# Performance work log

Hardware: AMD Instinct MI355X
Metric: run time of the kernel (lower is better)

Reference implementation:

```python
import jax, jax.numpy as jnp
import numpy as np

B, T, E, H = 2, 2048, 1024, 16
HS = E // H  # head size = 64
EPS = 1e-5


def setup_inputs() -> dict:
    key = jax.random.key(0)
    ks = jax.random.split(key, 12)
    s_e = 1.0 / np.sqrt(E)
    s_4e = 1.0 / np.sqrt(4 * E)
    return {
        "x": jax.random.normal(ks[0], (B, T, E), dtype=jnp.float32),
        # per-head projections (no bias), stacked over heads: [H, E, HS]
        "Wq": jax.random.uniform(ks[1], (H, E, HS), jnp.float32, -s_e, s_e),
        "Wk": jax.random.uniform(ks[2], (H, E, HS), jnp.float32, -s_e, s_e),
        "Wv": jax.random.uniform(ks[3], (H, E, HS), jnp.float32, -s_e, s_e),
        # output projection
        "Wo": jax.random.uniform(ks[4], (E, E), jnp.float32, -s_e, s_e),
        "bo": jax.random.uniform(ks[5], (E,), jnp.float32, -s_e, s_e),
        # feed-forward
        "W1": jax.random.uniform(ks[6], (E, 4 * E), jnp.float32, -s_e, s_e),
        "b1": jax.random.uniform(ks[7], (4 * E,), jnp.float32, -s_e, s_e),
        "W2": jax.random.uniform(ks[8], (4 * E, E), jnp.float32, -s_4e, s_4e),
        "b2": jax.random.uniform(ks[9], (E,), jnp.float32, -s_4e, s_4e),
        # layernorms
        "g1": jnp.ones((E,), jnp.float32),
        "be1": jnp.zeros((E,), jnp.float32),
        "g2": jnp.ones((E,), jnp.float32),
        "be2": jnp.zeros((E,), jnp.float32),
    }


def _layernorm(x, g, b):
    mu = jnp.mean(x, axis=-1, keepdims=True)
    var = jnp.var(x, axis=-1, keepdims=True)
    return (x - mu) * jax.lax.rsqrt(var + EPS) * g + b


def reference(x, Wq, Wk, Wv, Wo, bo, W1, b1, W2, b2, g1, be1, g2, be2):
    Bx, Tx, Ex = x.shape
    # --- multi-head causal self-attention (dropout = identity in eval) ---
    q = jnp.einsum("bte,hed->bhtd", x, Wq)
    k = jnp.einsum("bte,hed->bhtd", x, Wk)
    v = jnp.einsum("bte,hed->bhtd", x, Wv)
    scale = HS ** -0.5
    scores = jnp.einsum("bhtd,bhsd->bhts", q, k) * scale  # [B,H,T,T]
    causal = jnp.tril(jnp.ones((Tx, Tx), dtype=bool))
    scores = jnp.where(causal, scores, -jnp.inf)
    att = jax.nn.softmax(scores, axis=-1)
    out = jnp.einsum("bhts,bhsd->bhtd", att, v)  # [B,H,T,HS]
    out = out.transpose(0, 2, 1, 3).reshape(Bx, Tx, Ex)  # concat heads
    out = out @ Wo + bo
    # --- residual + LN1 ---
    x = _layernorm(x + out, g1, be1)
    # --- feed-forward ---
    h = jax.nn.relu(x @ W1 + b1)
    ff = h @ W2 + b2
    # --- residual + LN2 ---
    return _layernorm(x + ff, g2, be2)
```

## Files before the change

kernel.cpp:

```cpp
#include <hip/hip_runtime.h>
#include <hip/hip_bf16.h>
#include <cstdint>
#include <cstddef>

typedef __hip_bfloat16 bf16;
typedef __attribute__((ext_vector_type(8))) short short8;
typedef __attribute__((ext_vector_type(4))) float f32x4;

#define B_  2
#define T_  2048
#define E_  1024
#define H_  16
#define HS_ 64
#define EPS_ 1e-5f
#define NEG_BIG -1.0e30f

__device__ __forceinline__ float b2f(bf16 v) { return __bfloat162float(v); }
__device__ __forceinline__ bf16  f2b(float v) { return __float2bfloat16(v); }
__device__ __forceinline__ ushort f2bs(float v) { bf16 b = __float2bfloat16(v); return *(ushort*)&b; }
__device__ __forceinline__ float ld1(const bf16* p) { return b2f(*p); }
__device__ __forceinline__ float ld1(const float* p) { return *p; }
__device__ __forceinline__ void st1(bf16* p, float v) { *p = f2b(v); }
__device__ __forceinline__ void st1(float* p, float v) { *p = v; }

__device__ __forceinline__ void gload16(const void* g, const void* l) {
    __builtin_amdgcn_global_load_lds(
        (const __attribute__((address_space(1))) unsigned int*)(size_t)g,
        (__attribute__((address_space(3))) unsigned int*)(unsigned int)(size_t)l,
        16, 0, 0);
}

__device__ __forceinline__ void transpose_tile_s(short t[64][72],
                                                 const float* in, size_t ldin,
                                                 bf16* out, size_t ldout,
                                                 int r0, int c0)
{
    const int tid = threadIdx.x;
    const int tr = tid >> 2, tc4 = (tid & 3) * 16;

    const float* p = in + (size_t)(r0 + tr) * ldin + c0 + tc4;
    float4 v0 = ((const float4*)p)[0], v1 = ((const float4*)p)[1];
    float4 v2 = ((const float4*)p)[2], v3 = ((const float4*)p)[3];
    union { ushort u[16]; uint4 q[2]; } pk;
    pk.u[0] = f2bs(v0.x); pk.u[1] = f2bs(v0.y); pk.u[2]  = f2bs(v0.z); pk.u[3]  = f2bs(v0.w);
    pk.u[4] = f2bs(v1.x); pk.u[5] = f2bs(v1.y); pk.u[6]  = f2bs(v1.z); pk.u[7]  = f2bs(v1.w);
    pk.u[8] = f2bs(v2.x); pk.u[9] = f2bs(v2.y); pk.u[10] = f2bs(v2.z); pk.u[11] = f2bs(v2.w);
    pk.u[12] = f2bs(v3.x); pk.u[13] = f2bs(v3.y); pk.u[14] = f2bs(v3.z); pk.u[15] = f2bs(v3.w);
    *(uint4*)&t[tr][tc4]     = pk.q[0];
    *(uint4*)&t[tr][tc4 + 8] = pk.q[1];
    __syncthreads();

    const int tcI = tid >> 2, rj = (tid & 3) * 16;
    union { ushort u[16]; uint4 q[2]; } po;
    #pragma unroll
    for (int j = 0; j < 16; j++) po.u[j] = (ushort)t[rj + j][tcI];
    bf16* op = out + (size_t)(c0 + tcI) * ldout + r0 + rj;
    ((uint4*)op)[0] = po.q[0];
    ((uint4*)op)[1] = po.q[1];
}

__global__ __launch_bounds__(256) void prep_kernel(const float* __restrict__ x,
                                                   ushort* __restrict__ xb,
                                                   const float* __restrict__ Wq,
                                                   const float* __restrict__ Wk,
                                                   const float* __restrict__ Wv,
                                                   bf16* __restrict__ WqkvT,
                                                   const float* __restrict__ Wo,
                                                   bf16* __restrict__ WoT)
{
    __shared__ short t[64][72];
    const int bid = blockIdx.x;
    if (bid < 2048) {
        int i = (bid * 256 + (int)threadIdx.x) * 8;
        float4 a = ((const float4*)(x + i))[0];
        float4 b = ((const float4*)(x + i))[1];
        union { ushort u[8]; uint4 v; } p;
        p.u[0] = f2bs(a.x); p.u[1] = f2bs(a.y); p.u[2] = f2bs(a.z); p.u[3] = f2bs(a.w);
        p.u[4] = f2bs(b.x); p.u[5] = f2bs(b.y); p.u[6] = f2bs(b.z); p.u[7] = f2bs(b.w);
        *(uint4*)(xb + i) = p.v;
    } else if (bid < 2048 + 768) {
        const int i = bid - 2048;
        const int s = i >> 4, xt = i & 15;
        const int proj = s >> 4, h = s & 15;
        const float* W = (proj == 0) ? Wq : ((proj == 1) ? Wk : Wv);
        transpose_tile_s(t, W + (size_t)h * E_ * HS_, HS_,
                         WqkvT + ((size_t)proj * E_ + h * 64) * E_, E_,
                         xt * 64, 0);
    } else {
        const int i = bid - 2816;
        transpose_tile_s(t, Wo, E_, WoT, E_, (i >> 4) * 64, (i & 15) * 64);
    }
}

__global__ __launch_bounds__(256) void prep2_kernel(const float* __restrict__ W1,
                                                    bf16* __restrict__ W1T,
                                                    const float* __restrict__ W2,
                                                    bf16* __restrict__ W2T)
{
    __shared__ short t[64][72];
    const int bid = blockIdx.x;
    if (bid < 1024) {
        transpose_tile_s(t, W1, 4 * E_, W1T, E_,
                         (bid & 15) * 64, (bid >> 4) * 64);
    } else {
        const int i = bid - 1024;
        transpose_tile_s(t, W2, E_, W2T, 4 * E_,
                         (i >> 4) * 64, (i & 15) * 64);
    }
}

__global__ __launch_bounds__(256) void vt_transpose(const bf16* __restrict__ qkv,
                                                    bf16* __restrict__ vT)
{
    __shared__ short t[64][72];
    const int tid = threadIdx.x;
    const int bh  = blockIdx.y;
    const int b   = bh >> 4, h = bh & 15;
    const int t0  = blockIdx.x * 64;

    const bf16* in = qkv + ((size_t)b * T_) * (3 * E_) + 2 * E_ + h * 64;
    const int tr = tid >> 2, tc4 = (tid & 3) * 16;
    const bf16* p = in + (size_t)(t0 + tr) * (3 * E_) + tc4;
    uint4 q0 = ((const uint4*)p)[0];
    uint4 q1 = ((const uint4*)p)[1];
    *(uint4*)&t[tr][tc4]     = q0;
    *(uint4*)&t[tr][tc4 + 8] = q1;
    __syncthreads();

    const int tcI = tid >> 2, rj = (tid & 3) * 16;
    union { ushort u[16]; uint4 q[2]; } po;
    #pragma unroll
    for (int j = 0; j < 16; j++) po.u[j] = (ushort)t[rj + j][tcI];
    bf16* op = vT + ((size_t)bh * 64 + tcI) * T_ + t0 + rj;
    ((uint4*)op)[0] = po.q[0];
    ((uint4*)op)[1] = po.q[1];
}

template <int WROWS, int WCOLS, int MF, int NF, int KS, bool BIAS, bool RELU,
          typename TO>
__global__ __launch_bounds__(256) void gemm_bt(const bf16* __restrict__ A,
                                               const bf16* __restrict__ BT,
                                               const float* __restrict__ bias,
                                               TO* __restrict__ C,
                                               int M, int N, int K)
{
    constexpr int BM = WROWS * MF * 16;
    constexpr int BN = WCOLS * NF * 16;
    __shared__ short Asm[KS][BM][32];
    __shared__ short Bsm[KS][BN][32];

    const int tid  = threadIdx.x;
    const int wv   = tid >> 6, lane = tid & 63;
    const int quad = lane >> 4, l16 = lane & 15;
    const int row0 = blockIdx.y * BM, col0 = blockIdx.x * BN;
    const int mr0  = (wv / WCOLS) * MF * 16;
    const int nc0  = (wv % WCOLS) * NF * 16;

    const int sr = tid >> 2, sc = tid & 3;
    const bf16* Ag = A  + (size_t)(row0 + sr) * K + sc * 8;
    const bf16* Bg = BT + (size_t)(col0 + (sr % BN)) * K + sc * 8;

    f32x4 acc[MF][NF];
    #pragma unroll
    for (int i = 0; i < MF; i++)
        #pragma unroll
        for (int j = 0; j < NF; j++) acc[i][j] = (f32x4){0.f, 0.f, 0.f, 0.f};

    for (int kt = 0; kt < K; kt += 32 * KS) {
        __syncthreads();
        #pragma unroll
        for (int g = 0; g < KS; g++) {
            #pragma unroll
            for (int l = 0; l < BM / 64; l++)
                gload16(Ag + g * 32 + (size_t)l * 64 * K, &Asm[g][l * 64 + wv * 16][0]);
            #pragma unroll
            for (int l = 0; l < BN / 64; l++)
                gload16(Bg + g * 32 + (size_t)l * 64 * K, &Bsm[g][l * 64 + wv * 16][0]);
        }
        Ag += 32 * KS; Bg += 32 * KS;
        __syncthreads();

        #pragma unroll
        for (int g = 0; g < KS; g++) {
            short8 af[MF], bfr[NF];
            #pragma unroll
            for (int mf = 0; mf < MF; mf++)
                af[mf] = *(const short8*)&Asm[g][mr0 + mf * 16 + l16][quad * 8];
            #pragma unroll
            for (int nf = 0; nf < NF; nf++)
                bfr[nf] = *(const short8*)&Bsm[g][nc0 + nf * 16 + l16][quad * 8];
            #pragma unroll
            for (int mf = 0; mf < MF; mf++)
                #pragma unroll
                for (int nf = 0; nf < NF; nf++)
                    acc[mf][nf] = __builtin_amdgcn_mfma_f32_16x16x32_bf16(
                        af[mf], bfr[nf], acc[mf][nf], 0, 0, 0);
        }
    }

    #pragma unroll
    for (int nf = 0; nf < NF; nf++) {
        const int col = col0 + nc0 + nf * 16 + l16;
        const float bv = BIAS ? bias[col] : 0.f;
        #pragma unroll
        for (int mf = 0; mf < MF; mf++) {
            #pragma unroll
            for (int r = 0; r < 4; r++) {
                const int row = row0 + mr0 + mf * 16 + quad * 4 + r;
                float v = acc[mf][nf][r] + bv;
                if (RELU) v = fmaxf(v, 0.f);
                st1(&C[(size_t)row * N + col], v);
            }
        }
    }
}

__global__ __launch_bounds__(256) void attn_mfma(const bf16* __restrict__ qkv,
                                                 const bf16* __restrict__ vT,
                                                 bf16* __restrict__ outp)
{
    __shared__ short Klds[128][72];
    __shared__ short Vlds[64][136];
    __shared__ short Plds[4][16][136];

    const int tid  = threadIdx.x;
    const int w    = tid >> 6, lane = tid & 63;
    const int quad = lane >> 4, l16 = lane & 15;
    const int bh   = blockIdx.y;
    const int b    = bh >> 4, h = bh & 15;
    const size_t rowb = (size_t)b * T_ * 3 * E_;

    const int kkey = tid >> 1, kdh = (tid & 1) * 32;
    const bf16* Kg = qkv + rowb + E_ + h * HS_ + kdh;
    const int vd = tid >> 2, vseg = (tid & 3) * 32;
    const bf16* Vg = vT + ((size_t)bh * 64 + vd) * T_ + vseg;

    for (int pass = 0; pass < 2; pass++) {
        const int t0 = (pass == 0 ? blockIdx.x : 31 - blockIdx.x) * 64;
        const int qbase = t0 + w * 16;

        const bf16* Qp = qkv + rowb + (size_t)(qbase + l16) * (3 * E_) + h * HS_;
        const short8 aq0 = *(const short8*)(Qp + quad * 8);
        const short8 aq1 = *(const short8*)(Qp + 32 + quad * 8);

        f32x4 o[4];
        float mrow[4], lrow[4];
        #pragma unroll
        for (int f = 0; f < 4; f++) o[f] = (f32x4){0.f, 0.f, 0.f, 0.f};
        #pragma unroll
        for (int r = 0; r < 4; r++) { mrow[r] = NEG_BIG; lrow[r] = 0.f; }

        for (int kt0 = 0; kt0 <= t0; kt0 += 128) {
            __syncthreads();
            {
                const int kr = (kt0 + kkey < T_) ? kt0 + kkey : T_ - 1;
                const bf16* kp = Kg + (size_t)kr * (3 * E_);
                *(uint4*)&Klds[kkey][kdh]      = ((const uint4*)kp)[0];
                *(uint4*)&Klds[kkey][kdh + 8]  = ((const uint4*)kp)[1];
                *(uint4*)&Klds[kkey][kdh + 16] = ((const uint4*)kp)[2];
                *(uint4*)&Klds[kkey][kdh + 24] = ((const uint4*)kp)[3];
                const bf16* vp = Vg + kt0;
                *(uint4*)&Vlds[vd][vseg]       = ((const uint4*)vp)[0];
                *(uint4*)&Vlds[vd][vseg + 8]   = ((const uint4*)vp)[1];
                *(uint4*)&Vlds[vd][vseg + 16]  = ((const uint4*)vp)[2];
                *(uint4*)&Vlds[vd][vseg + 24]  = ((const uint4*)vp)[3];
            }
            __syncthreads();

            const bool active = (kt0 <= qbase + 15);
            const int nv0 = ((qbase + 15 - kt0) >> 4) + 1;
            const int nvalid = active ? (nv0 < 8 ? nv0 : 8) : 0;

            float p[8][4];
            #pragma unroll
            for (int c = 0; c < 8; c++) {
                if (c < nvalid) {
                    const int kc = kt0 + c * 16;
                    const int krow = c * 16 + l16;
                    short8 bk0 = *(const short8*)&Klds[krow][quad * 8];
                    short8 bk1 = *(const short8*)&Klds[krow][32 + quad * 8];
                    f32x4 s = (f32x4){0.f, 0.f, 0.f, 0.f};
                    s = __builtin_amdgcn_mfma_f32_16x16x32_bf16(aq0, bk0, s, 0, 0, 0);
                    s = __builtin_amdgcn_mfma_f32_16x16x32_bf16(aq1, bk1, s, 0, 0, 0);
                    const int key = kc + l16;
                    #pragma unroll
                    for (int r = 0; r < 4; r++) {
                        float sv = s[r] * 0.125f;
                        if (kc + 15 > qbase && key > qbase + quad * 4 + r)
                            sv = NEG_BIG;
                        p[c][r] = sv;
                    }
                }
            }
            if (active) {
                float mx[4];
                #pragma unroll
                for (int r = 0; r < 4; r++) mx[r] = p[0][r];
                #pragma unroll
                for (int c = 1; c < 8; c++)
                    if (c < nvalid)
                        #pragma unroll
                        for (int r = 0; r < 4; r++) mx[r] = fmaxf(mx[r], p[c][r]);
                #pragma unroll
                for (int off = 1; off < 16; off <<= 1)
                    #pragma unroll
                    for (int r = 0; r < 4; r++)
                        mx[r] = fmaxf(mx[r], __shfl_xor(mx[r], off));
                float alpha[4], rs[4];
                #pragma unroll
                for (int r = 0; r < 4; r++) {
                    const float mnew = fmaxf(mrow[r], mx[r]);
                    alpha[r] = __expf(mrow[r] - mnew);
                    mrow[r] = mnew;
                    rs[r] = 0.f;
                    #pragma unroll
                    for (int c = 0; c < 8; c++) {
                        p[c][r] = (c < nvalid) ? __expf(p[c][r] - mnew) : 0.f;
                        rs[r] += p[c][r];
                    }
                }
                #pragma unroll
                for (int off = 1; off < 16; off <<= 1)
                    #pragma unroll
                    for (int r = 0; r < 4; r++)
                        rs[r] += __shfl_xor(rs[r], off);
                #pragma unroll
                for (int r = 0; r < 4; r++) {
                    lrow[r] = lrow[r] * alpha[r] + rs[r];
                    #pragma unroll
                    for (int f = 0; f < 4; f++) o[f][r] *= alpha[r];
                }
                #pragma unroll
                for (int c = 0; c < 8; c++)
                    #pragma unroll
                    for (int r = 0; r < 4; r++)
                        Plds[w][quad * 4 + r][c * 16 + l16] = (short)f2bs(p[c][r]);
            }
            if (active) {
                #pragma unroll
                for (int kg = 0; kg < 4; kg++) {
                    short8 pa = *(const short8*)&Plds[w][l16][kg * 32 + quad * 8];
                    #pragma unroll
                    for (int f = 0; f < 4; f++) {
                        short8 vb = *(const short8*)&Vlds[f * 16 + l16][kg * 32 + quad * 8];
                        o[f] = __builtin_amdgcn_mfma_f32_16x16x32_bf16(pa, vb, o[f], 0, 0, 0);
                    }
                }
            }
        }

        #pragma unroll
        for (int r = 0; r < 4; r++) {
            const float linv = 1.f / lrow[r];
            bf16* op = outp + (size_t)(b * T_ + qbase + quad * 4 + r) * E_ + h * HS_;
            #pragma unroll
            for (int f = 0; f < 4; f++)
                op[f * 16 + l16] = f2b(o[f][r] * linv);
        }
    }
}

template <typename TA, typename TR, typename TO>
__global__ __launch_bounds__(256) void ln_kernel(const TA* a,
                                                 const TR* r,
                                                 const float* g,
                                                 const float* be,
                                                 TO* out)
{
    const int row = blockIdx.x;
    const TA* pa = a + (size_t)row * E_;
    const TR* pr = r + (size_t)row * E_;
    TO* po = out + (size_t)row * E_;

    float v[4];
    float sum = 0.f, sq = 0.f;
    #pragma unroll
    for (int j = 0; j < 4; j++) {
        int c = threadIdx.x + j * 256;
        v[j] = ld1(pa + c) + ld1(pr + c);
        sum += v[j];
        sq  += v[j] * v[j];
    }
    #pragma unroll
    for (int o = 32; o >= 1; o >>= 1) {
        sum += __shfl_xor(sum, o);
        sq  += __shfl_xor(sq, o);
    }
    __shared__ float red[8];
    const int wave = threadIdx.x >> 6, lane = threadIdx.x & 63;
    if (lane == 0) { red[wave] = sum; red[4 + wave] = sq; }
    __syncthreads();
    sum = red[0] + red[1] + red[2] + red[3];
    sq  = red[4] + red[5] + red[6] + red[7];

    const float mu  = sum * (1.f / E_);
    const float var = fmaxf(sq * (1.f / E_) - mu * mu, 0.f);
    const float rs  = rsqrtf(var + EPS_);

    #pragma unroll
    for (int j = 0; j < 4; j++) {
        int c = threadIdx.x + j * 256;
        st1(po + c, (v[j] - mu) * rs * g[c] + be[c]);
    }
}

extern "C" void kernel_launch(void* const* d_in, const int* in_sizes, int n_in,
                              void* d_out, int out_size, void* d_ws, size_t ws_size,
                              hipStream_t stream)
{
    (void)in_sizes; (void)n_in; (void)out_size; (void)ws_size;
    const float* x   = (const float*)d_in[0];
    const float* Wq  = (const float*)d_in[1];
    const float* Wk  = (const float*)d_in[2];
    const float* Wv  = (const float*)d_in[3];
    const float* Wo  = (const float*)d_in[4];
    const float* bo  = (const float*)d_in[5];
    const float* W1  = (const float*)d_in[6];
    const float* b1  = (const float*)d_in[7];
    const float* W2  = (const float*)d_in[8];
    const float* b2  = (const float*)d_in[9];
    const float* g1  = (const float*)d_in[10];
    const float* be1 = (const float*)d_in[11];
    const float* g2  = (const float*)d_in[12];
    const float* be2 = (const float*)d_in[13];

    const int M = B_ * T_;
    char* ws = (char*)d_ws;
    bf16* WqkvT = (bf16*)(ws);
    bf16* qkv   = (bf16*)(ws + (size_t)6291456);
    bf16* WoT   = (bf16*)(ws + (size_t)31457280);
    bf16* W1T   = (bf16*)(ws);
    bf16* W2T   = (bf16*)(ws + (size_t)8388608);
    bf16* proj  = (bf16*)(ws + (size_t)16777216);
    bf16* y     = (bf16*)(ws + (size_t)25165824);
    bf16* ff    = (bf16*)(ws + (size_t)16777216);

    bf16*  xb      = (bf16*)d_out;
    bf16*  vT      = (bf16*)d_out;
    bf16*  attnout = (bf16*)((char*)d_out + (size_t)8388608);
    bf16*  hbuf    = (bf16*)d_out;
    float* outf    = (float*)d_out;

    prep_kernel<<<3072, 256, 0, stream>>>(x, (ushort*)xb, Wq, Wk, Wv, WqkvT, Wo, WoT);

    gemm_bt<2, 2, 4, 4, 2, false, false, bf16><<<dim3(24, 32), 256, 0, stream>>>(
        xb, WqkvT, nullptr, qkv, M, 3 * E_, E_);

    vt_transpose<<<dim3(T_ / 64, B_ * H_), 256, 0, stream>>>(qkv, vT);

    attn_mfma<<<dim3(16, B_ * H_), 256, 0, stream>>>(qkv, vT, attnout);

    prep2_kernel<<<2048, 256, 0, stream>>>(W1, W1T, W2, W2T);

    gemm_bt<2, 2, 4, 2, 2, true, false, bf16><<<dim3(16, 32), 256, 0, stream>>>(
        attnout, WoT, bo, proj, M, E_, E_);

    ln_kernel<float, bf16, bf16><<<M, 256, 0, stream>>>(x, proj, g1, be1, y);

    for (int half = 0; half < 2; half++) {
        const size_t r0 = (size_t)half * 2048;
        gemm_bt<2, 2, 4, 4, 2, true, true, bf16><<<dim3(32, 16), 256, 0, stream>>>(
            y + r0 * E_, W1T, b1, hbuf, 2048, 4 * E_, E_);
        gemm_bt<2, 2, 2, 2, 2, true, false, bf16><<<dim3(16, 32), 256, 0, stream>>>(
            hbuf, W2T, b2, ff + r0 * E_, 2048, E_, 4 * E_);
    }

    ln_kernel<bf16, bf16, float><<<M, 256, 0, stream>>>(y, ff, g2, be2, outf);
}
```

Before: 415.3 us.

## Restructure causal attention: per-tile blocks, K/V register prefetch, exp2 softmax, MFMA row sums

```diff
diff --git a/kernel.cpp b/kernel.cpp
--- a/kernel.cpp
+++ b/kernel.cpp
@@ -14,6 +14,7 @@
 #define HS_ 64
 #define EPS_ 1e-5f
 #define NEG_BIG -1.0e30f
+#define SCL2E 0.18033688011112042f
 
 __device__ __forceinline__ float b2f(bf16 v) { return __bfloat162float(v); }
 __device__ __forceinline__ bf16  f2b(float v) { return __float2bfloat16(v); }
@@ -22,6 +23,14 @@
 __device__ __forceinline__ float ld1(const float* p) { return *p; }
 __device__ __forceinline__ void st1(bf16* p, float v) { *p = f2b(v); }
 __device__ __forceinline__ void st1(float* p, float v) { *p = v; }
+
+__device__ __forceinline__ float fexp2(float x) {
+#if __has_builtin(__builtin_amdgcn_exp2f)
+    return __builtin_amdgcn_exp2f(x);
+#else
+    return exp2f(x);
+#endif
+}
 
 __device__ __forceinline__ void gload16(const void* g, const void* l) {
     __builtin_amdgcn_global_load_lds(
@@ -215,9 +224,9 @@
     }
 }
 
-__global__ __launch_bounds__(256) void attn_mfma(const bf16* __restrict__ qkv,
-                                                 const bf16* __restrict__ vT,
-                                                 bf16* __restrict__ outp)
+__global__ __launch_bounds__(256, 3) void attn_mfma(const bf16* __restrict__ qkv,
+                                                    const bf16* __restrict__ vT,
+                                                    bf16* __restrict__ outp)
 {
     __shared__ short Klds[128][72];
     __shared__ short Vlds[64][136];
@@ -226,137 +235,142 @@
     const int tid  = threadIdx.x;
     const int w    = tid >> 6, lane = tid & 63;
     const int quad = lane >> 4, l16 = lane & 15;
-    const int bh   = blockIdx.y;
+
+    const int p    = blockIdx.y * 32 + blockIdx.x;
+    const int bh   = (p & 7) * 4 + ((p >> 3) & 3);
+    const int tile = 31 - (p >> 5);
     const int b    = bh >> 4, h = bh & 15;
     const size_t rowb = (size_t)b * T_ * 3 * E_;
+    const int t0    = tile * 64;
+    const int qbase = t0 + w * 16;
 
     const int kkey = tid >> 1, kdh = (tid & 1) * 32;
     const bf16* Kg = qkv + rowb + E_ + h * HS_ + kdh;
     const int vd = tid >> 2, vseg = (tid & 3) * 32;
-    const bf16* Vg = vT + ((size_t)bh * 64 + vd) * T_ + vseg;
-
-    for (int pass = 0; pass < 2; pass++) {
-        const int t0 = (pass == 0 ? blockIdx.x : 31 - blockIdx.x) * 64;
-        const int qbase = t0 + w * 16;
-
-        const bf16* Qp = qkv + rowb + (size_t)(qbase + l16) * (3 * E_) + h * HS_;
-        const short8 aq0 = *(const short8*)(Qp + quad * 8);
-        const short8 aq1 = *(const short8*)(Qp + 32 + quad * 8);
-
-        f32x4 o[4];
-        float mrow[4], lrow[4];
-        #pragma unroll
-        for (int f = 0; f < 4; f++) o[f] = (f32x4){0.f, 0.f, 0.f, 0.f};
-        #pragma unroll
-        for (int r = 0; r < 4; r++) { mrow[r] = NEG_BIG; lrow[r] = 0.f; }
-
-        for (int kt0 = 0; kt0 <= t0; kt0 += 128) {
-            __syncthreads();
-            {
-                const int kr = (kt0 + kkey < T_) ? kt0 + kkey : T_ - 1;
-                const bf16* kp = Kg + (size_t)kr * (3 * E_);
-                *(uint4*)&Klds[kkey][kdh]      = ((const uint4*)kp)[0];
-                *(uint4*)&Klds[kkey][kdh + 8]  = ((const uint4*)kp)[1];
-                *(uint4*)&Klds[kkey][kdh + 16] = ((const uint4*)kp)[2];
-                *(uint4*)&Klds[kkey][kdh + 24] = ((const uint4*)kp)[3];
-                const bf16* vp = Vg + kt0;
-                *(uint4*)&Vlds[vd][vseg]       = ((const uint4*)vp)[0];
-                *(uint4*)&Vlds[vd][vseg + 8]   = ((const uint4*)vp)[1];
-                *(uint4*)&Vlds[vd][vseg + 16]  = ((const uint4*)vp)[2];
-                *(uint4*)&Vlds[vd][vseg + 24]  = ((const uint4*)vp)[3];
-            }
-            __syncthreads();
-
-            const bool active = (kt0 <= qbase + 15);
-            const int nv0 = ((qbase + 15 - kt0) >> 4) + 1;
-            const int nvalid = active ? (nv0 < 8 ? nv0 : 8) : 0;
-
-            float p[8][4];
-            #pragma unroll
-            for (int c = 0; c < 8; c++) {
-                if (c < nvalid) {
-                    const int kc = kt0 + c * 16;
-                    const int krow = c * 16 + l16;
-                    short8 bk0 = *(const short8*)&Klds[krow][quad * 8];
-                    short8 bk1 = *(const short8*)&Klds[krow][32 + quad * 8];
-                    f32x4 s = (f32x4){0.f, 0.f, 0.f, 0.f};
-                    s = __builtin_amdgcn_mfma_f32_16x16x32_bf16(aq0, bk0, s, 0, 0, 0);
-                    s = __builtin_amdgcn_mfma_f32_16x16x32_bf16(aq1, bk1, s, 0, 0, 0);
-                    const int key = kc + l16;
-                    #pragma unroll
-                    for (int r = 0; r < 4; r++) {
-                        float sv = s[r] * 0.125f;
-                        if (kc + 15 > qbase && key > qbase + quad * 4 + r)
-                            sv = NEG_BIG;
-                        p[c][r] = sv;
-                    }
+    const bf16* Vg = vT + ((size_t)bh * 64 + vd) * T_;
+
+    const bf16* Qp = qkv + rowb + (size_t)(qbase + l16) * (3 * E_) + h * HS_;
+    const short8 aq0 = *(const short8*)(Qp + quad * 8);
+    const short8 aq1 = *(const short8*)(Qp + 32 + quad * 8);
+
+    short8 vone;
+    #pragma unroll
+    for (int j = 0; j < 8; j++) vone[j] = (short)0x3F80;
+
+    f32x4 o[4], o4;
+    #pragma unroll
+    for (int f = 0; f < 4; f++) o[f] = (f32x4){0.f, 0.f, 0.f, 0.f};
+    o4 = (f32x4){0.f, 0.f, 0.f, 0.f};
+    float mrow = NEG_BIG;
+
+    uint4 kq[4], vq[4];
+    auto ldKV = [&](int kt) {
+        const int krr = kt + kkey;
+        const int kr = (krr < T_) ? krr : T_ - 1;
+        const bf16* kp = Kg + (size_t)kr * (3 * E_);
+        #pragma unroll
+        for (int i = 0; i < 4; i++) kq[i] = ((const uint4*)kp)[i];
+        #pragma unroll
+        for (int i = 0; i < 4; i++) {
+            int col = kt + vseg + i * 8;
+            col = (col < T_ - 8) ? col : T_ - 8;
+            vq[i] = *(const uint4*)(Vg + col);
+        }
+    };
+
+    ldKV(0);
+    for (int kt0 = 0; kt0 <= t0; kt0 += 128) {
+        __syncthreads();
+        #pragma unroll
+        for (int i = 0; i < 4; i++) *(uint4*)&Klds[kkey][kdh + i * 8] = kq[i];
+        #pragma unroll
+        for (int i = 0; i < 4; i++) *(uint4*)&Vlds[vd][vseg + i * 8] = vq[i];
+        __syncthreads();
+        if (kt0 + 128 <= t0) ldKV(kt0 + 128);
+
+        const int nv0 = ((qbase + 15 - kt0) >> 4) + 1;
+        const int nvalid = nv0 < 8 ? nv0 : 8;
+
+        float ps[8][4];
+        #pragma unroll
+        for (int c = 0; c < 8; c++) {
+            if (c < nvalid) {
+                const int krow = c * 16 + l16;
+                short8 bk0 = *(const short8*)&Klds[krow][quad * 8];
+                short8 bk1 = *(const short8*)&Klds[krow][32 + quad * 8];
+                f32x4 s = (f32x4){0.f, 0.f, 0.f, 0.f};
+                s = __builtin_amdgcn_mfma_f32_16x16x32_bf16(bk0, aq0, s, 0, 0, 0);
+                s = __builtin_amdgcn_mfma_f32_16x16x32_bf16(bk1, aq1, s, 0, 0, 0);
+                const int kc = kt0 + c * 16;
+                const bool needmask = (kc + 15 > qbase);
+                #pragma unroll
+                for (int r = 0; r < 4; r++) {
+                    float sv = s[r] * SCL2E;
+                    if (needmask && (kc + quad * 4 + r > qbase + l16)) sv = NEG_BIG;
+                    ps[c][r] = sv;
                 }
             }
-            if (active) {
-                float mx[4];
+        }
+
+        float mx = ps[0][0];
+        #pragma unroll
+        for (int r = 1; r < 4; r++) mx = fmaxf(mx, ps[0][r]);
+        #pragma unroll
+        for (int c = 1; c < 8; c++)
+            if (c < nvalid)
                 #pragma unroll
-                for (int r = 0; r < 4; r++) mx[r] = p[0][r];
-                #pragma unroll
-                for (int c = 1; c < 8; c++)
-                    if (c < nvalid)
-                        #pragma unroll
-                        for (int r = 0; r < 4; r++) mx[r] = fmaxf(mx[r], p[c][r]);
-                #pragma unroll
-                for (int off = 1; off < 16; off <<= 1)
-                    #pragma unroll
-                    for (int r = 0; r < 4; r++)
-                        mx[r] = fmaxf(mx[r], __shfl_xor(mx[r], off));
-                float alpha[4], rs[4];
-                #pragma unroll
-                for (int r = 0; r < 4; r++) {
-                    const float mnew = fmaxf(mrow[r], mx[r]);
-                    alpha[r] = __expf(mrow[r] - mnew);
-                    mrow[r] = mnew;
-                    rs[r] = 0.f;
-                    #pragma unroll
-                    for (int c = 0; c < 8; c++) {
-                        p[c][r] = (c < nvalid) ? __expf(p[c][r] - mnew) : 0.f;
-                        rs[r] += p[c][r];
-                    }
-                }
-                #pragma unroll
-                for (int off = 1; off < 16; off <<= 1)
-                    #pragma unroll
-                    for (int r = 0; r < 4; r++)
-                        rs[r] += __shfl_xor(rs[r], off);
-                #pragma unroll
-                for (int r = 0; r < 4; r++) {
-                    lrow[r] = lrow[r] * alpha[r] + rs[r];
-                    #pragma unroll
-                    for (int f = 0; f < 4; f++) o[f][r] *= alpha[r];
-                }
-                #pragma unroll
-                for (int c = 0; c < 8; c++)
-                    #pragma unroll
-                    for (int r = 0; r < 4; r++)
-                        Plds[w][quad * 4 + r][c * 16 + l16] = (short)f2bs(p[c][r]);
+                for (int r = 0; r < 4; r++) mx = fmaxf(mx, ps[c][r]);
+        mx = fmaxf(mx, __shfl_xor(mx, 16));
+        mx = fmaxf(mx, __shfl_xor(mx, 32));
+        const float mnew = fmaxf(mrow, mx);
+        const float al = fexp2(mrow - mnew);
+        mrow = mnew;
+
+        #pragma unroll
+        for (int c = 0; c < 8; c++) {
+            uint2 pk; pk.x = 0u; pk.y = 0u;
+            if (c < nvalid) {
+                const float e0 = fexp2(ps[c][0] - mnew);
+                const float e1 = fexp2(ps[c][1] - mnew);
+                const float e2 = fexp2(ps[c][2] - mnew);
+                const float e3 = fexp2(ps[c][3] - mnew);
+                pk.x = (uint)f2bs(e0) | ((uint)f2bs(e1) << 16);
+                pk.y = (uint)f2bs(e2) | ((uint)f2bs(e3) << 16);
             }
-            if (active) {
-                #pragma unroll
-                for (int kg = 0; kg < 4; kg++) {
-                    short8 pa = *(const short8*)&Plds[w][l16][kg * 32 + quad * 8];
-                    #pragma unroll
-                    for (int f = 0; f < 4; f++) {
-                        short8 vb = *(const short8*)&Vlds[f * 16 + l16][kg * 32 + quad * 8];
-                        o[f] = __builtin_amdgcn_mfma_f32_16x16x32_bf16(pa, vb, o[f], 0, 0, 0);
-                    }
-                }
+            *(uint2*)&Plds[w][l16][c * 16 + quad * 4] = pk;
+        }
+
+        float alo[4];
+        #pragma unroll
+        for (int r = 0; r < 4; r++) alo[r] = __shfl(al, quad * 4 + r);
+        #pragma unroll
+        for (int f = 0; f < 4; f++)
+            #pragma unroll
+            for (int r = 0; r < 4; r++) o[f][r] *= alo[r];
+        #pragma unroll
+        for (int r = 0; r < 4; r++) o4[r] *= alo[r];
+
+        __builtin_amdgcn_s_setprio(1);
+        #pragma unroll
+        for (int kg = 0; kg < 4; kg++) {
+            short8 pa = *(const short8*)&Plds[w][l16][kg * 32 + quad * 8];
+            #pragma unroll
+            for (int f = 0; f < 4; f++) {
+                short8 vb = *(const short8*)&Vlds[f * 16 + l16][kg * 32 + quad * 8];
+                o[f] = __builtin_amdgcn_mfma_f32_16x16x32_bf16(pa, vb, o[f], 0, 0, 0);
             }
-        }
-
-        #pragma unroll
-        for (int r = 0; r < 4; r++) {
-            const float linv = 1.f / lrow[r];
-            bf16* op = outp + (size_t)(b * T_ + qbase + quad * 4 + r) * E_ + h * HS_;
-            #pragma unroll
-            for (int f = 0; f < 4; f++)
-                op[f * 16 + l16] = f2b(o[f][r] * linv);
-        }
+            o4 = __builtin_amdgcn_mfma_f32_16x16x32_bf16(pa, vone, o4, 0, 0, 0);
+        }
+        __builtin_amdgcn_s_setprio(0);
+    }
+
+    #pragma unroll
+    for (int r = 0; r < 4; r++) {
+        const float linv = 1.f / o4[r];
+        bf16* op = outp + (size_t)(b * T_ + qbase + quad * 4 + r) * E_ + h * HS_;
+        #pragma unroll
+        for (int f = 0; f < 4; f++)
+            op[f * 16 + l16] = f2b(o[f][r] * linv);
     }
 }
 
@@ -448,7 +462,7 @@
 
     vt_transpose<<<dim3(T_ / 64, B_ * H_), 256, 0, stream>>>(qkv, vT);
 
-    attn_mfma<<<dim3(16, B_ * H_), 256, 0, stream>>>(qkv, vT, attnout);
+    attn_mfma<<<dim3(32, 32), 256, 0, stream>>>(qkv, vT, attnout);
 
     prep2_kernel<<<2048, 256, 0, stream>>>(W1, W1T, W2, W2T);
 
```

New measurement: 447.8 us. 1.08x slower.
